# Kernel optimization log

Hardware: AMD Instinct MI355X
Metric: run time of the kernel (lower is better)

Reference implementation:

```python
import jax, jax.numpy as jnp
import numpy as np

N, M, D = 20000, 16000, 128

def setup_inputs() -> dict:
    key = jax.random.key(0)
    ks = jax.random.split(key, 4)
    return {
        "clear_feature": jax.random.normal(ks[0], (N, D), dtype=jnp.float32),
        "rain_feature": jax.random.normal(ks[1], (M, D), dtype=jnp.float32),
        # torch nn.Linear weight layout: (out_features, in_features)
        "W1": jax.random.normal(ks[2], (D, 2 * D), dtype=jnp.float32) * 0.05,
        "b1": jnp.zeros((D,), dtype=jnp.float32),
        "W2": jax.random.normal(ks[3], (1, D), dtype=jnp.float32) * 0.05,
        "b2": jnp.zeros((1,), dtype=jnp.float32),
    }

def reference(clear_feature, rain_feature, W1, b1, W2, b2):
    # --- KNN alignment (k=1): argmin of squared Euclidean distance == cdist+topk(smallest) ---
    x2 = jnp.sum(clear_feature * clear_feature, axis=-1, keepdims=True)   # [N,1]
    y2 = jnp.sum(rain_feature * rain_feature, axis=-1)                    # [M]
    d2 = x2 + y2 - 2.0 * (clear_feature @ rain_feature.T)                 # [N,M]
    idx = jnp.argmin(d2, axis=-1)                                         # [N]
    aligned = rain_feature[idx]                                           # [N,D] gather
    # --- attention MLP: Linear(2D->D) + ReLU + Linear(D->1) + Sigmoid ---
    comb = jnp.concatenate([clear_feature, aligned], axis=-1)             # [N,2D]
    h = jax.nn.relu(comb @ W1.T + b1)                                     # [N,D]
    w = jax.nn.sigmoid(h @ W2.T + b2)                                     # [N,1]
    # --- gated fusion ---
    return w * clear_feature + (1.0 - w) * aligned
```

## Files before the change

### kernel.cpp

```cpp
#include <hip/hip_runtime.h>
#include <stdint.h>

#define NN 20000
#define MM 16000
#define DD 128
#define CT 500
#define SPLITS 13
#define RB 79

typedef unsigned long long u64;
typedef _Float16 f16x8 __attribute__((ext_vector_type(8)));
typedef float f32x16 __attribute__((ext_vector_type(16)));

__global__ void k_init_keys(u64* keys) {
    int i = blockIdx.x * 256 + threadIdx.x;
    if (i < NN) keys[i] = ~0ull;
}

__global__ void k_y2(const float* __restrict__ rain, float* __restrict__ y2) {
    int row = blockIdx.x * 4 + (threadIdx.x >> 6);
    int lane = threadIdx.x & 63;
    if (row >= MM) return;
    float2 v = ((const float2*)(rain + (size_t)row * DD))[lane];
    float s = v.x * v.x + v.y * v.y;
    #pragma unroll
    for (int off = 32; off > 0; off >>= 1) s += __shfl_down(s, off);
    if (lane == 0) y2[row] = s;
}

__global__ void k_split_A(const float* __restrict__ clear_f,
                          _Float16* __restrict__ Ahi, _Float16* __restrict__ Alo) {
    int id = blockIdx.x * 256 + threadIdx.x;
    if (id >= NN * 16) return;
    int row = id >> 4, kc = id & 15;
    const float4* src = (const float4*)(clear_f + (size_t)row * DD + kc * 8);
    float4 v0 = src[0], v1 = src[1];
    float x[8] = {v0.x, v0.y, v0.z, v0.w, v1.x, v1.y, v1.z, v1.w};
    _Float16 hi[8], lo[8];
    #pragma unroll
    for (int j = 0; j < 8; ++j) {
        float s = -2.f * x[j];
        _Float16 h = (_Float16)s;
        hi[j] = h;
        lo[j] = (_Float16)(s - (float)h);
    }
    *(f16x8*)(Ahi + (size_t)row * DD + (size_t)kc * 8) = *(f16x8*)hi;
    *(f16x8*)(Alo + (size_t)row * DD + (size_t)kc * 8) = *(f16x8*)lo;
}

__global__ void k_split_B(const float* __restrict__ rain, _Float16* __restrict__ Bimg) {
    int id = blockIdx.x * 256 + threadIdx.x;
    if (id >= MM * 16) return;
    int cl = id & 31;
    int kp = (id >> 5) & 15;
    int tc = id >> 9;
    int row = tc * 32 + cl;
    const float4* src = (const float4*)(rain + (size_t)row * DD + kp * 8);
    float4 v0 = src[0], v1 = src[1];
    float x[8] = {v0.x, v0.y, v0.z, v0.w, v1.x, v1.y, v1.z, v1.w};
    _Float16 hi[8], lo[8];
    #pragma unroll
    for (int j = 0; j < 8; ++j) {
        _Float16 h = (_Float16)x[j];
        hi[j] = h;
        lo[j] = (_Float16)(x[j] - (float)h);
    }
    size_t base = (size_t)tc * 8192;
    int chunk = kp * 32 + cl;
    *(f16x8*)(Bimg + base + (size_t)chunk * 8) = *(f16x8*)hi;
    *(f16x8*)(Bimg + base + 4096 + (size_t)chunk * 8) = *(f16x8*)lo;
}

__global__ __launch_bounds__(256, 2) void k_dist(
        const _Float16* __restrict__ Ahi, const _Float16* __restrict__ Alo,
        const _Float16* __restrict__ Bimg, const float* __restrict__ y2,
        u64* __restrict__ keys) {
    __shared__ _Float16 lds[2][8192];

    const int tid = threadIdx.x;
    const int w = tid >> 6, lane = tid & 63;
    const int l5 = lane >> 5, l31 = lane & 31;
    const int split = blockIdx.y;
    const int n0 = blockIdx.x * 256;

    f16x8 afh0[8], afl0[8], afh1[8], afl1[8];
    {
        int r0 = n0 + w * 64 + l31;       if (r0 >= NN) r0 = NN - 1;
        int r1 = n0 + w * 64 + 32 + l31;  if (r1 >= NN) r1 = NN - 1;
        const _Float16* h0 = Ahi + (size_t)r0 * DD + l5 * 8;
        const _Float16* o0 = Alo + (size_t)r0 * DD + l5 * 8;
        const _Float16* h1 = Ahi + (size_t)r1 * DD + l5 * 8;
        const _Float16* o1 = Alo + (size_t)r1 * DD + l5 * 8;
        #pragma unroll
        for (int ks = 0; ks < 8; ++ks) {
            afh0[ks] = *(const f16x8*)(h0 + ks * 16);
            afl0[ks] = *(const f16x8*)(o0 + ks * 16);
            afh1[ks] = *(const f16x8*)(h1 + ks * 16);
            afl1[ks] = *(const f16x8*)(o1 + ks * 16);
        }
    }

    float bestd[32];
    int bestcol[32];
    #pragma unroll
    for (int s = 0; s < 32; ++s) { bestd[s] = 1e30f; bestcol[s] = 0; }

    const int nt = (CT - split + SPLITS - 1) / SPLITS;

    {
        const _Float16* gsrc = Bimg + (size_t)split * 8192;
        #pragma unroll
        for (int n = 0; n < 4; ++n) {
            int seg = w * 4 + n;
            __builtin_amdgcn_global_load_lds(
                (const __attribute__((address_space(1))) unsigned int*)
                    (gsrc + (size_t)seg * 512 + (size_t)lane * 8),
                (__attribute__((address_space(3))) unsigned int*)
                    (&lds[0][0] + (size_t)seg * 512),
                16, 0, 0);
        }
    }
    __syncthreads();

    int p = 0;
    for (int i = 0; i < nt; ++i) {
        const int t = split + i * SPLITS;

        if (i + 1 < nt) {
            const _Float16* gsrc = Bimg + (size_t)(t + SPLITS) * 8192;
            _Float16* lbase = &lds[1 - p][0];
            #pragma unroll
            for (int n = 0; n < 4; ++n) {
                int seg = w * 4 + n;
                __builtin_amdgcn_global_load_lds(
                    (const __attribute__((address_space(1))) unsigned int*)
                        (gsrc + (size_t)seg * 512 + (size_t)lane * 8),
                    (__attribute__((address_space(3))) unsigned int*)
                        (lbase + (size_t)seg * 512),
                    16, 0, 0);
            }
        }

        float y2v = y2[t * 32 + l31];

        f32x16 acc0, acc1;
        #pragma unroll
        for (int e = 0; e < 16; ++e) { acc0[e] = 0.f; acc1[e] = 0.f; }

        const _Float16* lbuf = &lds[p][0];
        #pragma unroll
        for (int ks = 0; ks < 8; ++ks) {
            f16x8 bh = *(const f16x8*)(lbuf + (size_t)ks * 512 + (size_t)lane * 8);
            f16x8 bl = *(const f16x8*)(lbuf + 4096 + (size_t)ks * 512 + (size_t)lane * 8);
            acc0 = __builtin_amdgcn_mfma_f32_32x32x16_f16(afh0[ks], bh, acc0, 0, 0, 0);
            acc1 = __builtin_amdgcn_mfma_f32_32x32x16_f16(afh1[ks], bh, acc1, 0, 0, 0);
            acc0 = __builtin_amdgcn_mfma_f32_32x32x16_f16(afh0[ks], bl, acc0, 0, 0, 0);
            acc1 = __builtin_amdgcn_mfma_f32_32x32x16_f16(afh1[ks], bl, acc1, 0, 0, 0);
            acc0 = __builtin_amdgcn_mfma_f32_32x32x16_f16(afl0[ks], bh, acc0, 0, 0, 0);
            acc1 = __builtin_amdgcn_mfma_f32_32x32x16_f16(afl1[ks], bh, acc1, 0, 0, 0);
        }

        int col = t * 32 + l31;
        #pragma unroll
        for (int e = 0; e < 16; ++e) {
            float d0 = acc0[e] + y2v;
            bool u0 = d0 < bestd[e];
            bestd[e] = u0 ? d0 : bestd[e];
            bestcol[e] = u0 ? col : bestcol[e];
            float d1 = acc1[e] + y2v;
            bool u1 = d1 < bestd[16 + e];
            bestd[16 + e] = u1 ? d1 : bestd[16 + e];
            bestcol[16 + e] = u1 ? col : bestcol[16 + e];
        }

        __syncthreads();
        p ^= 1;
    }

    #pragma unroll
    for (int s = 0; s < 32; ++s) {
        unsigned u = __float_as_uint(bestd[s]);
        u = (u & 0x80000000u) ? ~u : (u | 0x80000000u);
        u64 key = ((u64)u << 32) | (unsigned)bestcol[s];
        #pragma unroll
        for (int off = 1; off < 32; off <<= 1) {
            u64 o = __shfl_xor(key, off);
            if (o < key) key = o;
        }
        if (l31 == 0) {
            int e = s & 15, rb = s >> 4;
            int grow = n0 + w * 64 + rb * 32 + (e & 3) + 8 * (e >> 2) + 4 * l5;
            if (grow < NN) atomicMin(&keys[grow], key);
        }
    }
}

__global__ __launch_bounds__(256) void k_mlp(const float* __restrict__ clear_f,
                                             const float* __restrict__ rain_f,
                                             const float* __restrict__ W1,
                                             const float* __restrict__ b1,
                                             const float* __restrict__ W2,
                                             const float* __restrict__ b2,
                                             const u64* __restrict__ keys,
                                             float* __restrict__ out) {
    __shared__ float comb_s[16][260];
    __shared__ float w1_s[64][133];
    __shared__ float red_s[16][17];
    __shared__ float w_s[16];

    const int tid = threadIdx.x;
    const int n0 = blockIdx.x * 16;

    {
        int r = tid >> 4;
        int t = tid & 15;
        int n = n0 + r;
        unsigned idx = (unsigned)(keys[n] & 0xffffffffu);
        const float4* cp = (const float4*)(clear_f + (size_t)n * DD);
        const float4* rp = (const float4*)(rain_f + (size_t)idx * DD);
        *(float4*)&comb_s[r][4 * t] = cp[t];
        *(float4*)&comb_s[r][4 * (t + 16)] = cp[t + 16];
        *(float4*)&comb_s[r][DD + 4 * t] = rp[t];
        *(float4*)&comb_s[r][DD + 4 * (t + 16)] = rp[t + 16];
    }

    const int r = tid & 15;
    const int g = tid >> 4;
    const int d8 = g * 8;
    float h[8] = {};
    for (int kt = 0; kt < 4; ++kt) {
        __syncthreads();
        #pragma unroll
        for (int i = 0; i < 32; ++i) {
            int lin = i * 256 + tid;
            int kk = lin & 63;
            int d = lin >> 6;
            w1_s[kk][d] = W1[(size_t)d * 256 + kt * 64 + kk];
        }
        __syncthreads();
        #pragma unroll
        for (int kk = 0; kk < 64; ++kk) {
            float c = comb_s[r][kt * 64 + kk];
            float4 wa = *(const float4*)&w1_s[kk][d8];
            float4 wb = *(const float4*)&w1_s[kk][d8 + 4];
            h[0] = fmaf(c, wa.x, h[0]);
            h[1] = fmaf(c, wa.y, h[1]);
            h[2] = fmaf(c, wa.z, h[2]);
            h[3] = fmaf(c, wa.w, h[3]);
            h[4] = fmaf(c, wb.x, h[4]);
            h[5] = fmaf(c, wb.y, h[5]);
            h[6] = fmaf(c, wb.z, h[6]);
            h[7] = fmaf(c, wb.w, h[7]);
        }
    }
    float part = 0.f;
    #pragma unroll
    for (int j = 0; j < 8; ++j) {
        float hv = h[j] + b1[d8 + j];
        hv = hv > 0.f ? hv : 0.f;
        part = fmaf(hv, W2[d8 + j], part);
    }
    red_s[r][g] = part;
    __syncthreads();
    if (tid < 16) {
        float s = 0.f;
        #pragma unroll
        for (int g2 = 0; g2 < 16; ++g2) s += red_s[tid][g2];
        s += b2[0];
        w_s[tid] = 1.f / (1.f + expf(-s));
    }
    __syncthreads();
    {
        int rw = tid >> 4;
        int c8 = (tid & 15) * 8;
        float wv = w_s[rw];
        float ov[8];
        #pragma unroll
        for (int j = 0; j < 8; ++j) {
            float cv = comb_s[rw][c8 + j];
            float av = comb_s[rw][DD + c8 + j];
            ov[j] = wv * cv + (1.f - wv) * av;
        }
        float4* o = (float4*)(out + (size_t)(n0 + rw) * DD + c8);
        o[0] = make_float4(ov[0], ov[1], ov[2], ov[3]);
        o[1] = make_float4(ov[4], ov[5], ov[6], ov[7]);
    }
}

extern "C" void kernel_launch(void* const* d_in, const int* in_sizes, int n_in,
                              void* d_out, int out_size, void* d_ws, size_t ws_size,
                              hipStream_t stream) {
    const float* clear_f = (const float*)d_in[0];
    const float* rain_f = (const float*)d_in[1];
    const float* W1 = (const float*)d_in[2];
    const float* b1 = (const float*)d_in[3];
    const float* W2 = (const float*)d_in[4];
    const float* b2 = (const float*)d_in[5];
    float* out = (float*)d_out;

    char* ws = (char*)d_ws;
    u64* keys = (u64*)ws;
    float* y2 = (float*)(ws + 160000);
    _Float16* Ahi = (_Float16*)(ws + 224000);
    _Float16* Alo = (_Float16*)(ws + 5344000);
    _Float16* Bimg = (_Float16*)(ws + 10464000);

    k_init_keys<<<(NN + 255) / 256, 256, 0, stream>>>(keys);
    k_y2<<<MM / 4, 256, 0, stream>>>(rain_f, y2);
    k_split_A<<<(NN * 16 + 255) / 256, 256, 0, stream>>>(clear_f, Ahi, Alo);
    k_split_B<<<(MM * 16 + 255) / 256, 256, 0, stream>>>(rain_f, Bimg);
    k_dist<<<dim3(RB, SPLITS), 256, 0, stream>>>(Ahi, Alo, Bimg, y2, keys);
    k_mlp<<<NN / 16, 256, 0, stream>>>(clear_f, rain_f, W1, b1, W2, b2, keys, out);
}
```

Measured before the change: 393.5 us.

## Widen distance tiles, fuse A split, drop atomics, MFMA-based MLP

The distance kernel now processes 64-column B tiles per iteration and does the fp16 hi/lo split of the clear features inline, which removes the separate A-split kernel and its global round trip. It folds y2 into the accumulator init and keeps the argmin column as packed 4-bit indices to save registers. The global key init and atomicMin are replaced by per-split key writes followed by a reduce kernel. The MLP is rewritten to run the first linear layer on fp16 MFMA with a pre-laid-out W1 image, which adds fp16 rounding error to the gating weight.

```diff
diff --git a/kernel.cpp b/kernel.cpp
--- a/kernel.cpp
+++ b/kernel.cpp
@@ -4,18 +4,13 @@
 #define NN 20000
 #define MM 16000
 #define DD 128
-#define CT 500
-#define SPLITS 13
+#define CT2 250
+#define SPLITS 32
 #define RB 79
 
 typedef unsigned long long u64;
 typedef _Float16 f16x8 __attribute__((ext_vector_type(8)));
 typedef float f32x16 __attribute__((ext_vector_type(16)));
-
-__global__ void k_init_keys(u64* keys) {
-    int i = blockIdx.x * 256 + threadIdx.x;
-    if (i < NN) keys[i] = ~0ull;
-}
 
 __global__ void k_y2(const float* __restrict__ rain, float* __restrict__ y2) {
     int row = blockIdx.x * 4 + (threadIdx.x >> 6);
@@ -28,33 +23,14 @@
     if (lane == 0) y2[row] = s;
 }
 
-__global__ void k_split_A(const float* __restrict__ clear_f,
-                          _Float16* __restrict__ Ahi, _Float16* __restrict__ Alo) {
-    int id = blockIdx.x * 256 + threadIdx.x;
-    if (id >= NN * 16) return;
-    int row = id >> 4, kc = id & 15;
-    const float4* src = (const float4*)(clear_f + (size_t)row * DD + kc * 8);
-    float4 v0 = src[0], v1 = src[1];
-    float x[8] = {v0.x, v0.y, v0.z, v0.w, v1.x, v1.y, v1.z, v1.w};
-    _Float16 hi[8], lo[8];
-    #pragma unroll
-    for (int j = 0; j < 8; ++j) {
-        float s = -2.f * x[j];
-        _Float16 h = (_Float16)s;
-        hi[j] = h;
-        lo[j] = (_Float16)(s - (float)h);
-    }
-    *(f16x8*)(Ahi + (size_t)row * DD + (size_t)kc * 8) = *(f16x8*)hi;
-    *(f16x8*)(Alo + (size_t)row * DD + (size_t)kc * 8) = *(f16x8*)lo;
-}
-
 __global__ void k_split_B(const float* __restrict__ rain, _Float16* __restrict__ Bimg) {
     int id = blockIdx.x * 256 + threadIdx.x;
-    if (id >= MM * 16) return;
+    if (id >= CT2 * 1024) return;
     int cl = id & 31;
-    int kp = (id >> 5) & 15;
-    int tc = id >> 9;
-    int row = tc * 32 + cl;
+    int cg = (id >> 5) & 1;
+    int kp = (id >> 6) & 15;
+    int tc = id >> 10;
+    int row = tc * 64 + cg * 32 + cl;
     const float4* src = (const float4*)(rain + (size_t)row * DD + kp * 8);
     float4 v0 = src[0], v1 = src[1];
     float x[8] = {v0.x, v0.y, v0.z, v0.w, v1.x, v1.y, v1.z, v1.w};
@@ -65,53 +41,50 @@
         hi[j] = h;
         lo[j] = (_Float16)(x[j] - (float)h);
     }
-    size_t base = (size_t)tc * 8192;
-    int chunk = kp * 32 + cl;
+    int ks = kp >> 1, kh = kp & 1;
+    int chunk = ((ks * 2 + cg) * 2 + kh) * 32 + cl;
+    size_t base = (size_t)tc * 16384;
     *(f16x8*)(Bimg + base + (size_t)chunk * 8) = *(f16x8*)hi;
-    *(f16x8*)(Bimg + base + 4096 + (size_t)chunk * 8) = *(f16x8*)lo;
+    *(f16x8*)(Bimg + base + 8192 + (size_t)chunk * 8) = *(f16x8*)lo;
+}
+
+__global__ void k_w1img(const float* __restrict__ W1, _Float16* __restrict__ W1img) {
+    int id = blockIdx.x * 256 + threadIdx.x;
+    if (id >= 4096) return;
+    int cl = id & 31;
+    int kh = (id >> 5) & 1;
+    int cg = (id >> 6) & 3;
+    int ks = id >> 8;
+    int d = cg * 32 + cl;
+    int k = ks * 16 + kh * 8;
+    const float4* src = (const float4*)(W1 + (size_t)d * 256 + k);
+    float4 v0 = src[0], v1 = src[1];
+    float x[8] = {v0.x, v0.y, v0.z, v0.w, v1.x, v1.y, v1.z, v1.w};
+    _Float16 h[8];
+    #pragma unroll
+    for (int j = 0; j < 8; ++j) h[j] = (_Float16)x[j];
+    *(f16x8*)(W1img + (size_t)id * 8) = *(f16x8*)h;
 }
 
 __global__ __launch_bounds__(256, 2) void k_dist(
-        const _Float16* __restrict__ Ahi, const _Float16* __restrict__ Alo,
+        const float* __restrict__ clear_f,
         const _Float16* __restrict__ Bimg, const float* __restrict__ y2,
-        u64* __restrict__ keys) {
-    __shared__ _Float16 lds[2][8192];
+        u64* __restrict__ keys2) {
+    __shared__ _Float16 lds[2][16384];
 
     const int tid = threadIdx.x;
     const int w = tid >> 6, lane = tid & 63;
     const int l5 = lane >> 5, l31 = lane & 31;
-    const int split = blockIdx.y;
-    const int n0 = blockIdx.x * 256;
-
-    f16x8 afh0[8], afl0[8], afh1[8], afl1[8];
+    const int b = blockIdx.x;
+    const int split = b & 31;
+    const int n0 = (b >> 5) * 256;
+    const int nt = (CT2 - split + SPLITS - 1) / SPLITS;
+
     {
-        int r0 = n0 + w * 64 + l31;       if (r0 >= NN) r0 = NN - 1;
-        int r1 = n0 + w * 64 + 32 + l31;  if (r1 >= NN) r1 = NN - 1;
-        const _Float16* h0 = Ahi + (size_t)r0 * DD + l5 * 8;
-        const _Float16* o0 = Alo + (size_t)r0 * DD + l5 * 8;
-        const _Float16* h1 = Ahi + (size_t)r1 * DD + l5 * 8;
-        const _Float16* o1 = Alo + (size_t)r1 * DD + l5 * 8;
-        #pragma unroll
-        for (int ks = 0; ks < 8; ++ks) {
-            afh0[ks] = *(const f16x8*)(h0 + ks * 16);
-            afl0[ks] = *(const f16x8*)(o0 + ks * 16);
-            afh1[ks] = *(const f16x8*)(h1 + ks * 16);
-            afl1[ks] = *(const f16x8*)(o1 + ks * 16);
-        }
-    }
-
-    float bestd[32];
-    int bestcol[32];
-    #pragma unroll
-    for (int s = 0; s < 32; ++s) { bestd[s] = 1e30f; bestcol[s] = 0; }
-
-    const int nt = (CT - split + SPLITS - 1) / SPLITS;
-
-    {
-        const _Float16* gsrc = Bimg + (size_t)split * 8192;
-        #pragma unroll
-        for (int n = 0; n < 4; ++n) {
-            int seg = w * 4 + n;
+        const _Float16* gsrc = Bimg + (size_t)split * 16384;
+        #pragma unroll
+        for (int n = 0; n < 8; ++n) {
+            int seg = w * 8 + n;
             __builtin_amdgcn_global_load_lds(
                 (const __attribute__((address_space(1))) unsigned int*)
                     (gsrc + (size_t)seg * 512 + (size_t)lane * 8),
@@ -120,57 +93,112 @@
                 16, 0, 0);
         }
     }
+
+    f16x8 afh[2][8], afl[2][8];
+    #pragma unroll
+    for (int rb = 0; rb < 2; ++rb) {
+        int r = n0 + w * 64 + rb * 32 + l31;
+        if (r >= NN) r = NN - 1;
+        const float* ap = clear_f + (size_t)r * DD + l5 * 8;
+        #pragma unroll
+        for (int ks = 0; ks < 8; ++ks) {
+            float4 v0 = *(const float4*)(ap + ks * 16);
+            float4 v1 = *(const float4*)(ap + ks * 16 + 4);
+            float x[8] = {v0.x, v0.y, v0.z, v0.w, v1.x, v1.y, v1.z, v1.w};
+            _Float16 hi[8], lo[8];
+            #pragma unroll
+            for (int j = 0; j < 8; ++j) {
+                float s = -2.f * x[j];
+                _Float16 h = (_Float16)s;
+                hi[j] = h;
+                lo[j] = (_Float16)(s - (float)h);
+            }
+            afh[rb][ks] = *(f16x8*)hi;
+            afl[rb][ks] = *(f16x8*)lo;
+        }
+    }
     __syncthreads();
+
+    float bestd[32];
+    unsigned bits[4] = {0u, 0u, 0u, 0u};
+    #pragma unroll
+    for (int s = 0; s < 32; ++s) bestd[s] = 1e30f;
 
     int p = 0;
     for (int i = 0; i < nt; ++i) {
         const int t = split + i * SPLITS;
 
         if (i + 1 < nt) {
-            const _Float16* gsrc = Bimg + (size_t)(t + SPLITS) * 8192;
-            _Float16* lbase = &lds[1 - p][0];
+            const _Float16* gsrc = Bimg + (size_t)(t + SPLITS) * 16384;
+            _Float16* dst = &lds[1 - p][0];
             #pragma unroll
-            for (int n = 0; n < 4; ++n) {
-                int seg = w * 4 + n;
+            for (int n = 0; n < 8; ++n) {
+                int seg = w * 8 + n;
                 __builtin_amdgcn_global_load_lds(
                     (const __attribute__((address_space(1))) unsigned int*)
                         (gsrc + (size_t)seg * 512 + (size_t)lane * 8),
                     (__attribute__((address_space(3))) unsigned int*)
-                        (lbase + (size_t)seg * 512),
+                        (dst + (size_t)seg * 512),
                     16, 0, 0);
             }
         }
 
-        float y2v = y2[t * 32 + l31];
-
-        f32x16 acc0, acc1;
-        #pragma unroll
-        for (int e = 0; e < 16; ++e) { acc0[e] = 0.f; acc1[e] = 0.f; }
+        float y2v0 = y2[t * 64 + l31];
+        float y2v1 = y2[t * 64 + 32 + l31];
+
+        f32x16 acc00, acc01, acc10, acc11;
+        #pragma unroll
+        for (int e = 0; e < 16; ++e) {
+            acc00[e] = y2v0; acc10[e] = y2v0;
+            acc01[e] = y2v1; acc11[e] = y2v1;
+        }
 
         const _Float16* lbuf = &lds[p][0];
         #pragma unroll
         for (int ks = 0; ks < 8; ++ks) {
-            f16x8 bh = *(const f16x8*)(lbuf + (size_t)ks * 512 + (size_t)lane * 8);
-            f16x8 bl = *(const f16x8*)(lbuf + 4096 + (size_t)ks * 512 + (size_t)lane * 8);
-            acc0 = __builtin_amdgcn_mfma_f32_32x32x16_f16(afh0[ks], bh, acc0, 0, 0, 0);
-            acc1 = __builtin_amdgcn_mfma_f32_32x32x16_f16(afh1[ks], bh, acc1, 0, 0, 0);
-            acc0 = __builtin_amdgcn_mfma_f32_32x32x16_f16(afh0[ks], bl, acc0, 0, 0, 0);
-            acc1 = __builtin_amdgcn_mfma_f32_32x32x16_f16(afh1[ks], bl, acc1, 0, 0, 0);
-            acc0 = __builtin_amdgcn_mfma_f32_32x32x16_f16(afl0[ks], bh, acc0, 0, 0, 0);
-            acc1 = __builtin_amdgcn_mfma_f32_32x32x16_f16(afl1[ks], bh, acc1, 0, 0, 0);
-        }
-
-        int col = t * 32 + l31;
+            f16x8 bh0 = *(const f16x8*)(lbuf + (size_t)(ks * 2 + 0) * 512 + (size_t)lane * 8);
+            f16x8 bh1 = *(const f16x8*)(lbuf + (size_t)(ks * 2 + 1) * 512 + (size_t)lane * 8);
+            f16x8 bl0 = *(const f16x8*)(lbuf + 8192 + (size_t)(ks * 2 + 0) * 512 + (size_t)lane * 8);
+            f16x8 bl1 = *(const f16x8*)(lbuf + 8192 + (size_t)(ks * 2 + 1) * 512 + (size_t)lane * 8);
+            acc00 = __builtin_amdgcn_mfma_f32_32x32x16_f16(afh[0][ks], bh0, acc00, 0, 0, 0);
+            acc10 = __builtin_amdgcn_mfma_f32_32x32x16_f16(afh[1][ks], bh0, acc10, 0, 0, 0);
+            acc01 = __builtin_amdgcn_mfma_f32_32x32x16_f16(afh[0][ks], bh1, acc01, 0, 0, 0);
+            acc11 = __builtin_amdgcn_mfma_f32_32x32x16_f16(afh[1][ks], bh1, acc11, 0, 0, 0);
+            acc00 = __builtin_amdgcn_mfma_f32_32x32x16_f16(afh[0][ks], bl0, acc00, 0, 0, 0);
+            acc10 = __builtin_amdgcn_mfma_f32_32x32x16_f16(afh[1][ks], bl0, acc10, 0, 0, 0);
+            acc01 = __builtin_amdgcn_mfma_f32_32x32x16_f16(afh[0][ks], bl1, acc01, 0, 0, 0);
+            acc11 = __builtin_amdgcn_mfma_f32_32x32x16_f16(afh[1][ks], bl1, acc11, 0, 0, 0);
+            acc00 = __builtin_amdgcn_mfma_f32_32x32x16_f16(afl[0][ks], bh0, acc00, 0, 0, 0);
+            acc10 = __builtin_amdgcn_mfma_f32_32x32x16_f16(afl[1][ks], bh0, acc10, 0, 0, 0);
+            acc01 = __builtin_amdgcn_mfma_f32_32x32x16_f16(afl[0][ks], bh1, acc01, 0, 0, 0);
+            acc11 = __builtin_amdgcn_mfma_f32_32x32x16_f16(afl[1][ks], bh1, acc11, 0, 0, 0);
+        }
+
+        const unsigned ibase = (unsigned)i << 1;
         #pragma unroll
         for (int e = 0; e < 16; ++e) {
-            float d0 = acc0[e] + y2v;
-            bool u0 = d0 < bestd[e];
-            bestd[e] = u0 ? d0 : bestd[e];
-            bestcol[e] = u0 ? col : bestcol[e];
-            float d1 = acc1[e] + y2v;
-            bool u1 = d1 < bestd[16 + e];
-            bestd[16 + e] = u1 ? d1 : bestd[16 + e];
-            bestcol[16 + e] = u1 ? col : bestcol[16 + e];
+            {
+                float d0 = acc00[e], d1 = acc01[e];
+                bool tk = d1 < d0;
+                float dm = tk ? d1 : d0;
+                int s = e, sh = 4 * (e & 7);
+                bool up = dm < bestd[s];
+                bestd[s] = up ? dm : bestd[s];
+                unsigned nib = ibase | (unsigned)tk;
+                bits[s >> 3] = up ? ((bits[s >> 3] & ~(15u << sh)) | (nib << sh))
+                                  : bits[s >> 3];
+            }
+            {
+                float d0 = acc10[e], d1 = acc11[e];
+                bool tk = d1 < d0;
+                float dm = tk ? d1 : d0;
+                int s = 16 + e, sh = 4 * (s & 7);
+                bool up = dm < bestd[s];
+                bestd[s] = up ? dm : bestd[s];
+                unsigned nib = ibase | (unsigned)tk;
+                bits[s >> 3] = up ? ((bits[s >> 3] & ~(15u << sh)) | (nib << sh))
+                                  : bits[s >> 3];
+            }
         }
 
         __syncthreads();
@@ -179,9 +207,12 @@
 
     #pragma unroll
     for (int s = 0; s < 32; ++s) {
+        unsigned nib = (bits[s >> 3] >> (4 * (s & 7))) & 15u;
+        int i4 = (int)(nib >> 1), cg = (int)(nib & 1);
+        int col = (split + i4 * SPLITS) * 64 + cg * 32 + l31;
         unsigned u = __float_as_uint(bestd[s]);
         u = (u & 0x80000000u) ? ~u : (u | 0x80000000u);
-        u64 key = ((u64)u << 32) | (unsigned)bestcol[s];
+        u64 key = ((u64)u << 32) | (unsigned)col;
         #pragma unroll
         for (int off = 1; off < 32; off <<= 1) {
             u64 o = __shfl_xor(key, off);
@@ -190,100 +221,116 @@
         if (l31 == 0) {
             int e = s & 15, rb = s >> 4;
             int grow = n0 + w * 64 + rb * 32 + (e & 3) + 8 * (e >> 2) + 4 * l5;
-            if (grow < NN) atomicMin(&keys[grow], key);
-        }
-    }
-}
-
-__global__ __launch_bounds__(256) void k_mlp(const float* __restrict__ clear_f,
-                                             const float* __restrict__ rain_f,
-                                             const float* __restrict__ W1,
-                                             const float* __restrict__ b1,
-                                             const float* __restrict__ W2,
-                                             const float* __restrict__ b2,
-                                             const u64* __restrict__ keys,
-                                             float* __restrict__ out) {
-    __shared__ float comb_s[16][260];
-    __shared__ float w1_s[64][133];
-    __shared__ float red_s[16][17];
-    __shared__ float w_s[16];
+            if (grow < NN) keys2[(size_t)grow * SPLITS + split] = key;
+        }
+    }
+}
+
+__global__ void k_reduce(const u64* __restrict__ keys2, int* __restrict__ idx) {
+    int n = blockIdx.x * 256 + threadIdx.x;
+    if (n >= NN) return;
+    const u64* p = keys2 + (size_t)n * SPLITS;
+    u64 best = ~0ull;
+    #pragma unroll
+    for (int j = 0; j < SPLITS; ++j) {
+        u64 k = p[j];
+        if (k < best) best = k;
+    }
+    idx[n] = (int)(best & 0xffffffffu);
+}
+
+__global__ __launch_bounds__(256, 2) void k_mlp(
+        const float* __restrict__ clear_f, const float* __restrict__ rain_f,
+        const _Float16* __restrict__ W1img, const float* __restrict__ b1,
+        const float* __restrict__ W2, const float* __restrict__ b2,
+        const int* __restrict__ idx, float* __restrict__ out) {
+    __shared__ _Float16 w1s[32768];
 
     const int tid = threadIdx.x;
-    const int n0 = blockIdx.x * 16;
-
-    {
-        int r = tid >> 4;
-        int t = tid & 15;
-        int n = n0 + r;
-        unsigned idx = (unsigned)(keys[n] & 0xffffffffu);
-        const float4* cp = (const float4*)(clear_f + (size_t)n * DD);
-        const float4* rp = (const float4*)(rain_f + (size_t)idx * DD);
-        *(float4*)&comb_s[r][4 * t] = cp[t];
-        *(float4*)&comb_s[r][4 * (t + 16)] = cp[t + 16];
-        *(float4*)&comb_s[r][DD + 4 * t] = rp[t];
-        *(float4*)&comb_s[r][DD + 4 * (t + 16)] = rp[t + 16];
-    }
-
-    const int r = tid & 15;
-    const int g = tid >> 4;
-    const int d8 = g * 8;
-    float h[8] = {};
-    for (int kt = 0; kt < 4; ++kt) {
-        __syncthreads();
-        #pragma unroll
-        for (int i = 0; i < 32; ++i) {
-            int lin = i * 256 + tid;
-            int kk = lin & 63;
-            int d = lin >> 6;
-            w1_s[kk][d] = W1[(size_t)d * 256 + kt * 64 + kk];
-        }
-        __syncthreads();
-        #pragma unroll
-        for (int kk = 0; kk < 64; ++kk) {
-            float c = comb_s[r][kt * 64 + kk];
-            float4 wa = *(const float4*)&w1_s[kk][d8];
-            float4 wb = *(const float4*)&w1_s[kk][d8 + 4];
-            h[0] = fmaf(c, wa.x, h[0]);
-            h[1] = fmaf(c, wa.y, h[1]);
-            h[2] = fmaf(c, wa.z, h[2]);
-            h[3] = fmaf(c, wa.w, h[3]);
-            h[4] = fmaf(c, wb.x, h[4]);
-            h[5] = fmaf(c, wb.y, h[5]);
-            h[6] = fmaf(c, wb.z, h[6]);
-            h[7] = fmaf(c, wb.w, h[7]);
-        }
-    }
-    float part = 0.f;
-    #pragma unroll
-    for (int j = 0; j < 8; ++j) {
-        float hv = h[j] + b1[d8 + j];
-        hv = hv > 0.f ? hv : 0.f;
-        part = fmaf(hv, W2[d8 + j], part);
-    }
-    red_s[r][g] = part;
+    const int w = tid >> 6, lane = tid & 63;
+    const int l5 = lane >> 5, l31 = lane & 31;
+    const int n0 = blockIdx.x * 128;
+
+    #pragma unroll
+    for (int n = 0; n < 16; ++n) {
+        int seg = w * 16 + n;
+        __builtin_amdgcn_global_load_lds(
+            (const __attribute__((address_space(1))) unsigned int*)
+                (W1img + (size_t)seg * 512 + (size_t)lane * 8),
+            (__attribute__((address_space(3))) unsigned int*)
+                (&w1s[0] + (size_t)seg * 512),
+            16, 0, 0);
+    }
+
+    int n = n0 + w * 32 + l31;
+    int nc = n < NN ? n : NN - 1;
+    int rid = idx[nc];
+    f16x8 af[16];
+    #pragma unroll
+    for (int ks = 0; ks < 16; ++ks) {
+        int k0 = ks * 16 + l5 * 8;
+        const float4* src = (k0 < 128)
+            ? (const float4*)(clear_f + (size_t)nc * DD + k0)
+            : (const float4*)(rain_f + (size_t)rid * DD + (k0 - 128));
+        float4 v0 = src[0], v1 = src[1];
+        float x[8] = {v0.x, v0.y, v0.z, v0.w, v1.x, v1.y, v1.z, v1.w};
+        _Float16 h[8];
+        #pragma unroll
+        for (int j = 0; j < 8; ++j) h[j] = (_Float16)x[j];
+        af[ks] = *(f16x8*)h;
+    }
+
     __syncthreads();
-    if (tid < 16) {
-        float s = 0.f;
-        #pragma unroll
-        for (int g2 = 0; g2 < 16; ++g2) s += red_s[tid][g2];
-        s += b2[0];
-        w_s[tid] = 1.f / (1.f + expf(-s));
-    }
-    __syncthreads();
-    {
-        int rw = tid >> 4;
-        int c8 = (tid & 15) * 8;
-        float wv = w_s[rw];
-        float ov[8];
-        #pragma unroll
-        for (int j = 0; j < 8; ++j) {
-            float cv = comb_s[rw][c8 + j];
-            float av = comb_s[rw][DD + c8 + j];
-            ov[j] = wv * cv + (1.f - wv) * av;
-        }
-        float4* o = (float4*)(out + (size_t)(n0 + rw) * DD + c8);
-        o[0] = make_float4(ov[0], ov[1], ov[2], ov[3]);
-        o[1] = make_float4(ov[4], ov[5], ov[6], ov[7]);
+
+    f32x16 acc[4];
+    #pragma unroll
+    for (int cg = 0; cg < 4; ++cg)
+        #pragma unroll
+        for (int e = 0; e < 16; ++e) acc[cg][e] = 0.f;
+
+    #pragma unroll
+    for (int ks = 0; ks < 16; ++ks) {
+        #pragma unroll
+        for (int cg = 0; cg < 4; ++cg) {
+            f16x8 bh = *(const f16x8*)(&w1s[0] +
+                ((size_t)((ks * 4 + cg) * 2 + l5)) * 256 + (size_t)l31 * 8);
+            acc[cg] = __builtin_amdgcn_mfma_f32_32x32x16_f16(af[ks], bh, acc[cg], 0, 0, 0);
+        }
+    }
+
+    float b1v[4], w2v[4];
+    #pragma unroll
+    for (int cg = 0; cg < 4; ++cg) {
+        b1v[cg] = b1[cg * 32 + l31];
+        w2v[cg] = W2[cg * 32 + l31];
+    }
+    float b2v = b2[0];
+
+    #pragma unroll
+    for (int e = 0; e < 16; ++e) {
+        float part = 0.f;
+        #pragma unroll
+        for (int cg = 0; cg < 4; ++cg) {
+            float hv = acc[cg][e] + b1v[cg];
+            hv = hv > 0.f ? hv : 0.f;
+            part = fmaf(hv, w2v[cg], part);
+        }
+        #pragma unroll
+        for (int off = 1; off < 32; off <<= 1) part += __shfl_xor(part, off);
+        float s = part + b2v;
+        float wv = 1.f / (1.f + expf(-s));
+        int row = n0 + w * 32 + (e & 3) + 8 * (e >> 2) + 4 * l5;
+        if (row < NN) {
+            int rid2 = idx[row];
+            float4 cv = *(const float4*)(clear_f + (size_t)row * DD + l31 * 4);
+            float4 av = *(const float4*)(rain_f + (size_t)rid2 * DD + l31 * 4);
+            float4 ov;
+            ov.x = wv * cv.x + (1.f - wv) * av.x;
+            ov.y = wv * cv.y + (1.f - wv) * av.y;
+            ov.z = wv * cv.z + (1.f - wv) * av.z;
+            ov.w = wv * cv.w + (1.f - wv) * av.w;
+            *(float4*)(out + (size_t)row * DD + l31 * 4) = ov;
+        }
     }
 }
 
@@ -299,16 +346,16 @@
     float* out = (float*)d_out;
 
     char* ws = (char*)d_ws;
-    u64* keys = (u64*)ws;
-    float* y2 = (float*)(ws + 160000);
-    _Float16* Ahi = (_Float16*)(ws + 224000);
-    _Float16* Alo = (_Float16*)(ws + 5344000);
-    _Float16* Bimg = (_Float16*)(ws + 10464000);
-
-    k_init_keys<<<(NN + 255) / 256, 256, 0, stream>>>(keys);
+    u64* keys2 = (u64*)ws;
+    int* idx = (int*)(ws + 5120000);
+    float* y2 = (float*)(ws + 5200000);
+    _Float16* Bimg = (_Float16*)(ws + 5264000);
+    _Float16* W1img = (_Float16*)(ws + 13456000);
+
     k_y2<<<MM / 4, 256, 0, stream>>>(rain_f, y2);
-    k_split_A<<<(NN * 16 + 255) / 256, 256, 0, stream>>>(clear_f, Ahi, Alo);
-    k_split_B<<<(MM * 16 + 255) / 256, 256, 0, stream>>>(rain_f, Bimg);
-    k_dist<<<dim3(RB, SPLITS), 256, 0, stream>>>(Ahi, Alo, Bimg, y2, keys);
-    k_mlp<<<NN / 16, 256, 0, stream>>>(clear_f, rain_f, W1, b1, W2, b2, keys, out);
-}
+    k_split_B<<<(CT2 * 1024 + 255) / 256, 256, 0, stream>>>(rain_f, Bimg);
+    k_w1img<<<16, 256, 0, stream>>>(W1, W1img);
+    k_dist<<<RB * SPLITS, 256, 0, stream>>>(clear_f, Bimg, y2, keys2);
+    k_reduce<<<(NN + 255) / 256, 256, 0, stream>>>(keys2, idx);
+    k_mlp<<<(NN + 127) / 128, 256, 0, stream>>>(clear_f, rain_f, W1img, b1, W2, b2, idx, out);
+}
```

Measured after the change: 356.4 us. 9.4% less time.
